# Kernel optimization log

Hardware: AMD Instinct MI355X
Metric: run time of the kernel (lower is better)

## Reference

```python
import jax, jax.numpy as jnp
import numpy as np

T, B, C, H = 2048, 2, 1024, 16
DK = C // H


def setup_inputs() -> dict:
    key = jax.random.key(0)
    ks = jax.random.split(key, 12)
    s = 1.0 / np.sqrt(C)
    return {
        "query": jax.random.normal(ks[0], (T, B, C), jnp.float32),
        "key": jax.random.normal(ks[1], (T, B, C), jnp.float32),
        "value": jax.random.normal(ks[2], (T, B, C), jnp.float32),
        "Wq": jax.random.normal(ks[3], (C, C), jnp.float32) * s,
        "bq": jnp.zeros((C,), jnp.float32),
        "Wk": jax.random.normal(ks[4], (C, C), jnp.float32) * s,
        "bk": jnp.zeros((C,), jnp.float32),
        "Wv": jax.random.normal(ks[5], (C, C), jnp.float32) * s,
        "bv": jnp.zeros((C,), jnp.float32),
        "Wo": jax.random.normal(ks[6], (C, C), jnp.float32) * s,
        "bo": jnp.zeros((C,), jnp.float32),
        "key_padding_mask": jax.random.randint(ks[7], (B, T), 0, 2).astype(jnp.bool_),
    }


def reference(query, key, value, Wq, bq, Wk, bk, Wv, bv, Wo, bo, key_padding_mask):
    # T,B,C -> B,T,C
    q_in = jnp.transpose(query, (1, 0, 2))
    k_in = jnp.transpose(key, (1, 0, 2))
    v_in = jnp.transpose(value, (1, 0, 2))
    nb = q_in.shape[0]
    # linear projections, split heads: B,T,C -> B,H,T,dk
    def proj(x, W, b):
        y = x @ W.T + b
        return jnp.transpose(y.reshape(nb, -1, H, DK), (0, 2, 1, 3))
    q = proj(q_in, Wq, bq)
    k = proj(k_in, Wk, bk)
    v = proj(v_in, Wv, bv)
    # scores: B,H,T1,T2
    scores = jnp.einsum("bhqd,bhkd->bhqk", q, k) / np.sqrt(DK).astype(np.float32)
    scores = jnp.where(key_padding_mask[:, None, None, :], -jnp.inf, scores)
    attn = jax.nn.softmax(scores, axis=-1)
    # context: B,H,T1,dk -> B,T1,C
    x = jnp.einsum("bhqk,bhkd->bhqd", attn, v)
    x = jnp.transpose(x, (0, 2, 1, 3)).reshape(nb, -1, H * DK)
    out = x @ Wo.T + bo
    # B,T,C -> T,B,C
    return jnp.transpose(out, (1, 0, 2))
```

## Files before the change

kernel.cpp:

```cpp
#include <hip/hip_runtime.h>
#include <stdint.h>

typedef __attribute__((ext_vector_type(4))) float f32x4;
typedef __attribute__((ext_vector_type(16))) float f32x16;
typedef __attribute__((ext_vector_type(8))) short bf16x8;
typedef __attribute__((ext_vector_type(2))) unsigned int u32x2;
typedef __attribute__((ext_vector_type(4))) unsigned int u32x4;
typedef unsigned short u16;
typedef unsigned int u32;

#define DEVINL __device__ __forceinline__

DEVINL u16 f2bf(float f) {
  u32 u = __builtin_bit_cast(u32, f);
  u += 0x7FFFu + ((u >> 16) & 1u);
  return (u16)(u >> 16);
}

DEVINL float exp2_hw(float x) {
  float r;
  asm("v_exp_f32 %0, %1\n\ts_nop 0" : "=v"(r) : "v"(x));
  return r;
}

DEVINL u32 cvt_pk_bf16(float lo, float hi) {
  u32 r;
  asm("v_cvt_pk_bf16_f32 %0, %1, %2" : "=v"(r) : "v"(lo), "v"(hi));
  return r;
}

DEVINL void gload16(const void* g, void* l) {
  __builtin_amdgcn_global_load_lds((const __attribute__((address_space(1))) void*)g,
                                   (__attribute__((address_space(3))) void*)l, 16, 0, 0);
}

DEVINL void wait_vm0() { asm volatile("s_waitcnt vmcnt(0)" ::: "memory"); }
DEVINL void wait_vm3() { asm volatile("s_waitcnt vmcnt(3)" ::: "memory"); }
DEVINL void wait_vm4() { asm volatile("s_waitcnt vmcnt(4)" ::: "memory"); }
DEVINL void wait_vm6() { asm volatile("s_waitcnt vmcnt(6)" ::: "memory"); }

__global__ void cvt_w_mask(const float* __restrict__ wq, const float* __restrict__ wk,
                           const float* __restrict__ wv, const float* __restrict__ wo,
                           ushort4* __restrict__ dst,
                           const u32* __restrict__ mraw, float* __restrict__ mout) {
  if (blockIdx.x == 4096) {
    __shared__ int notint, notfloat;
    int tid = threadIdx.x;
    if (tid == 0) { notint = 0; notfloat = 0; }
    __syncthreads();
    for (int i = tid; i < 1024; i += 256) {
      u32 w = mraw[i];
      if (w != 0u && w != 1u) notint = 1;
      if (w != 0u && w != 0x3f800000u) notfloat = 1;
    }
    __syncthreads();
    bool words = (!notint) || (!notfloat);
    for (int i = tid; i < 4096; i += 256) {
      u32 v = words ? mraw[i] : (u32)(((const unsigned char*)mraw)[i]);
      mout[i] = v ? -1.0e38f : -8.0f;
    }
    return;
  }
  int i = blockIdx.x * 256 + threadIdx.x;
  float4 v4;
  if (i < 262144) v4 = ((const float4*)wq)[i];
  else if (i < 524288) v4 = ((const float4*)wk)[i - 262144];
  else if (i < 786432) v4 = ((const float4*)wv)[i - 524288];
  else v4 = ((const float4*)wo)[i - 786432];
  ushort4 o;
  o.x = f2bf(v4.x); o.y = f2bf(v4.y); o.z = f2bf(v4.z); o.w = f2bf(v4.w);
  dst[i] = o;
}

DEVINL void gemm_f32a_body(const float* __restrict__ A, const u16* __restrict__ W,
                           const float* __restrict__ bias, u16* __restrict__ out_bf,
                           int tile, int mode, float scale, float* Asf, u16* Bs) {
  const int tid = threadIdx.x, lane = tid & 63;
  const int wave = tid >> 6, wm = wave & 1, wn = wave >> 1;
  const int m0 = (tile >> 3) << 7;
  const int n0 = (tile & 7) << 7;
  const int l15 = lane & 15, l4 = lane >> 4;
  const f32x4 zero = {0.f, 0.f, 0.f, 0.f};
  f32x4 acc[4][4];
#pragma unroll
  for (int i = 0; i < 4; i++)
#pragma unroll
    for (int j = 0; j < 4; j++) acc[i][j] = zero;

  auto stage = [&](int buf, int kti) {
    float* Ab = Asf + buf * 4096;
    u16* Bb = Bs + buf * 4096;
#pragma unroll
    for (int it = 0; it < 4; ++it) {
      int c = tid + (it << 8);
      int row = c >> 3, qs = (c & 7) ^ (row & 7);
      gload16(A + (size_t)(m0 + row) * 1024 + kti * 32 + qs * 4, (void*)(Ab + c * 4));
    }
#pragma unroll
    for (int it = 0; it < 2; ++it) {
      int c = tid + (it << 8);
      int row = c >> 2, qs = (c & 3) ^ ((row & 3) ^ ((row >> 2) & 3));
      gload16(W + (size_t)(n0 + row) * 1024 + kti * 32 + qs * 8, (void*)(Bb + c * 8));
    }
  };

  stage(0, 0);

  for (int kti = 0; kti < 32; ++kti) {
    if (kti < 31) stage((kti + 1) & 1, kti + 1);
    if (kti == 31) wait_vm0(); else wait_vm6();
    __builtin_amdgcn_s_barrier();
    __builtin_amdgcn_sched_barrier(0);

    const float* Ac = Asf + (kti & 1) * 4096;
    const u16* Bc = Bs + (kti & 1) * 4096;
    bf16x8 af[4], bfr[4];
#pragma unroll
    for (int i = 0; i < 4; i++) {
      int ra = (wm << 6) + (i << 4) + l15;
      int sw = ra & 7;
      float4 v0 = *(const float4*)(Ac + ra * 32 + ((((l4 << 1) | 0) ^ sw) << 2));
      float4 v1 = *(const float4*)(Ac + ra * 32 + ((((l4 << 1) | 1) ^ sw) << 2));
      u32x4 aw = {cvt_pk_bf16(v0.x, v0.y), cvt_pk_bf16(v0.z, v0.w),
                  cvt_pk_bf16(v1.x, v1.y), cvt_pk_bf16(v1.z, v1.w)};
      af[i] = __builtin_bit_cast(bf16x8, aw);
      int rb = (wn << 6) + (i << 4) + l15;
      bfr[i] = *(const bf16x8*)(Bc + rb * 32 + ((l4 * 8) ^ ((((rb & 3) ^ ((rb >> 2) & 3))) << 3)));
    }
    __builtin_amdgcn_s_setprio(1);
#pragma unroll
    for (int i = 0; i < 4; i++)
#pragma unroll
      for (int j = 0; j < 4; j++)
        acc[i][j] = __builtin_amdgcn_mfma_f32_16x16x32_bf16(af[i], bfr[j], acc[i][j], 0, 0, 0);
    __builtin_amdgcn_s_setprio(0);
    if (kti < 31) __builtin_amdgcn_s_barrier();
  }

#pragma unroll
  for (int j = 0; j < 4; j++) {
    const int col = n0 + (wn << 6) + (j << 4) + l15;
    const float bc = bias[col];
#pragma unroll
    for (int i = 0; i < 4; i++) {
#pragma unroll
      for (int r = 0; r < 4; r++) {
        const int row = m0 + (wm << 6) + (i << 4) + (l4 << 2) + r;
        float v = (acc[i][j][r] + bc) * scale;
        int t = row >> 1, b2 = row & 1, h = col >> 6, dh = col & 63;
        if (mode == 2)
          out_bf[((size_t)(b2 * 16 + h) * 64 + dh) * 2048 + t] = f2bf(v);
        else
          out_bf[((size_t)(b2 * 16 + h) * 2048 + t) * 64 + dh] = f2bf(v);
      }
    }
  }
}

__global__ __launch_bounds__(256, 3) void gemm_qkv(
    const float* __restrict__ q_in, const float* __restrict__ k_in, const float* __restrict__ v_in,
    const u16* __restrict__ wq, const u16* __restrict__ wk, const u16* __restrict__ wv,
    const float* __restrict__ bq, const float* __restrict__ bk, const float* __restrict__ bv,
    u16* __restrict__ Qh, u16* __restrict__ Kh, u16* __restrict__ Vth) {
  __shared__ __align__(16) float Asf[2 * 4096];
  __shared__ __align__(16) u16 Bs[2 * 4096];
  const float C2 = 0.18033688011112042f;
  int wg = blockIdx.x;
  int swz = (wg & 7) * 96 + (wg >> 3);
  int prob = swz >> 8, tile = swz & 255;
  if (prob == 0)      gemm_f32a_body(q_in, wq, bq, Qh,  tile, 0, C2, Asf, Bs);
  else if (prob == 1) gemm_f32a_body(k_in, wk, bk, Kh,  tile, 0, 1.0f, Asf, Bs);
  else                gemm_f32a_body(v_in, wv, bv, Vth, tile, 2, 1.0f, Asf, Bs);
}

__global__ __launch_bounds__(256, 2) void gemm_o(
    const u16* __restrict__ ctx, const u16* __restrict__ wo,
    const float* __restrict__ bo, float* __restrict__ out) {
  __shared__ __align__(16) u16 As[3 * 2048];
  __shared__ __align__(16) u16 Bs[3 * 4096];
  const int tid = threadIdx.x, lane = tid & 63;
  const int wave = tid >> 6, wm = wave & 1, wn = wave >> 1;
  const int wg = blockIdx.x;
  const int swz = (wg & 7) * 64 + (wg >> 3);
  const int m0 = (swz >> 3) << 6;
  const int n0 = (swz & 7) << 7;
  const int l15 = lane & 15, l4 = lane >> 4;
  const f32x4 zero = {0.f, 0.f, 0.f, 0.f};
  f32x4 acc[2][4];
#pragma unroll
  for (int i = 0; i < 2; i++)
#pragma unroll
    for (int j = 0; j < 4; j++) acc[i][j] = zero;

  auto stage = [&](int buf, int kti) {
    u16* Ab = As + buf * 2048;
    u16* Bb = Bs + buf * 4096;
    {
      int c = tid;
      int row = c >> 2, qs = (c & 3) ^ ((row & 3) ^ ((row >> 2) & 3));
      gload16(ctx + (size_t)(m0 + row) * 1024 + kti * 32 + qs * 8, (void*)(Ab + c * 8));
    }
#pragma unroll
    for (int it = 0; it < 2; ++it) {
      int c = tid + (it << 8);
      int row = c >> 2, qs = (c & 3) ^ ((row & 3) ^ ((row >> 2) & 3));
      gload16(wo + (size_t)(n0 + row) * 1024 + kti * 32 + qs * 8, (void*)(Bb + c * 8));
    }
  };

  stage(0, 0);
  stage(1, 1);

  for (int kti = 0; kti < 32; ++kti) {
    const int cur = kti % 3;
    if (kti == 31) wait_vm0(); else wait_vm3();
    __builtin_amdgcn_s_barrier();
    __builtin_amdgcn_sched_barrier(0);
    if (kti < 30) stage((kti + 2) % 3, kti + 2);

    const u16* Ac = As + cur * 2048;
    const u16* Bc = Bs + cur * 4096;
    bf16x8 af[2], bfr[4];
#pragma unroll
    for (int i = 0; i < 2; i++) {
      int ra = (wm << 5) + (i << 4) + l15;
      af[i] = *(const bf16x8*)(Ac + ra * 32 + ((l4 * 8) ^ ((((ra & 3) ^ ((ra >> 2) & 3))) << 3)));
    }
#pragma unroll
    for (int j = 0; j < 4; j++) {
      int rb = (wn << 6) + (j << 4) + l15;
      bfr[j] = *(const bf16x8*)(Bc + rb * 32 + ((l4 * 8) ^ ((((rb & 3) ^ ((rb >> 2) & 3))) << 3)));
    }
    __builtin_amdgcn_s_setprio(1);
#pragma unroll
    for (int i = 0; i < 2; i++)
#pragma unroll
      for (int j = 0; j < 4; j++)
        acc[i][j] = __builtin_amdgcn_mfma_f32_16x16x32_bf16(af[i], bfr[j], acc[i][j], 0, 0, 0);
    __builtin_amdgcn_s_setprio(0);
  }

#pragma unroll
  for (int j = 0; j < 4; j++) {
    const int col = n0 + (wn << 6) + (j << 4) + l15;
    const float bc = bo[col];
#pragma unroll
    for (int i = 0; i < 2; i++) {
#pragma unroll
      for (int r = 0; r < 4; r++) {
        const int row = m0 + (wm << 5) + (i << 4) + (l4 << 2) + r;
        float v = acc[i][j][r] + bc;
        int t = row & 2047, b2 = row >> 11;
        out[(size_t)(t * 2 + b2) * 1024 + col] = v;
      }
    }
  }
}

__global__ __launch_bounds__(256, 2) void attn_fwd(
    const u16* __restrict__ Qh, const u16* __restrict__ Kh, const u16* __restrict__ Vt,
    const float* __restrict__ maskf, u16* __restrict__ ctx) {
  __shared__ __align__(16) u16 Ks[3][64 * 64];
  __shared__ __align__(16) u16 Vs[3][64 * 64];
  __shared__ __align__(16) float Ml[2048];
  const int tid = threadIdx.x, lane = tid & 63, wave = tid >> 6;
  const int wg = blockIdx.x;
  const int swz = (wg & 7) * 64 + (wg >> 3);
  const int qt = swz & 15, bh = swz >> 4;
  const int bb = bh >> 4, h = bh & 15;
  const int l31 = lane & 31, hi = lane >> 5;
  const size_t kvbase = (size_t)bh * 2048 * 64;
  const int qbase = qt * 128 + wave * 32;

  gload16(maskf + bb * 2048 + tid * 4, (void*)(&Ml[tid * 4]));
  gload16(maskf + bb * 2048 + 1024 + tid * 4, (void*)(&Ml[1024 + tid * 4]));

  bf16x8 qf[4];
#pragma unroll
  for (int kc = 0; kc < 4; kc++)
    qf[kc] = *(const bf16x8*)(Qh + kvbase + (size_t)(qbase + l31) * 64 + kc * 16 + hi * 8);

  f32x16 zz;
#pragma unroll
  for (int e = 0; e < 16; e++) zz[e] = 0.f;
  f32x16 O[2];
  O[0] = zz; O[1] = zz;
  float l_ = 0.f;

  auto stage = [&](int buf, int kt) {
#pragma unroll
    for (int it = 0; it < 2; ++it) {
      int c = tid + (it << 8);
      int row = c >> 3, qs = (c & 7) ^ (row & 7);
      gload16(Kh + kvbase + (size_t)(kt * 64 + row) * 64 + qs * 8, (void*)(&Ks[buf][c * 8]));
      gload16(Vt + kvbase + (size_t)row * 2048 + kt * 64 + qs * 8, (void*)(&Vs[buf][c * 8]));
    }
  };

  stage(0, 0);
  stage(1, 1);

  for (int kt = 0; kt < 32; ++kt) {
    const int cur = kt % 3;
    if (kt == 31) wait_vm0(); else wait_vm4();
    __builtin_amdgcn_s_barrier();
    __builtin_amdgcn_sched_barrier(0);
    if (kt < 30) stage((kt + 2) % 3, kt + 2);

    f32x16 s[2];
    s[0] = zz; s[1] = zz;
    __builtin_amdgcn_s_setprio(1);
#pragma unroll
    for (int kc = 0; kc < 4; kc++) {
      const int ch = (((kc * 2 + hi) ^ (l31 & 7)) << 3);
      bf16x8 kf0 = *(const bf16x8*)(&Ks[cur][l31 * 64 + ch]);
      bf16x8 kf1 = *(const bf16x8*)(&Ks[cur][(l31 + 32) * 64 + ch]);
      s[0] = __builtin_amdgcn_mfma_f32_32x32x16_bf16(kf0, qf[kc], s[0], 0, 0, 0);
      s[1] = __builtin_amdgcn_mfma_f32_32x32x16_bf16(kf1, qf[kc], s[1], 0, 0, 0);
    }
    __builtin_amdgcn_s_setprio(0);

    float rs = 0.f;
#pragma unroll
    for (int kb = 0; kb < 2; kb++)
#pragma unroll
      for (int g = 0; g < 4; g++) {
        float4 mv = *(const float4*)(&Ml[kt * 64 + kb * 32 + g * 8 + hi * 4]);
        float p0 = exp2_hw(s[kb][4 * g + 0] + mv.x);
        float p1 = exp2_hw(s[kb][4 * g + 1] + mv.y);
        float p2 = exp2_hw(s[kb][4 * g + 2] + mv.z);
        float p3 = exp2_hw(s[kb][4 * g + 3] + mv.w);
        s[kb][4 * g + 0] = p0; s[kb][4 * g + 1] = p1;
        s[kb][4 * g + 2] = p2; s[kb][4 * g + 3] = p3;
        rs += (p0 + p1) + (p2 + p3);
      }
    rs += __shfl_xor(rs, 32);
    l_ += rs;

    u32 pw[2][8];
#pragma unroll
    for (int kb = 0; kb < 2; kb++)
#pragma unroll
      for (int g = 0; g < 4; g++) {
        pw[kb][2 * g]     = cvt_pk_bf16(s[kb][4 * g + 0], s[kb][4 * g + 1]);
        pw[kb][2 * g + 1] = cvt_pk_bf16(s[kb][4 * g + 2], s[kb][4 * g + 3]);
      }

    __builtin_amdgcn_s_setprio(1);
#pragma unroll
    for (int kc = 0; kc < 4; kc++) {
      const int kb = kc >> 1, m = kc & 1;
      auto r0 = __builtin_amdgcn_permlane32_swap(pw[kb][4 * m + 0], pw[kb][4 * m + 2], false, false);
      auto r1 = __builtin_amdgcn_permlane32_swap(pw[kb][4 * m + 1], pw[kb][4 * m + 3], false, false);
      u32x4 fw = {r0[0], r1[0], r0[1], r1[1]};
      bf16x8 pf = __builtin_bit_cast(bf16x8, fw);
      const int ch = (((kc * 2 + hi) ^ (l31 & 7)) << 3);
      bf16x8 vf0 = *(const bf16x8*)(&Vs[cur][l31 * 64 + ch]);
      bf16x8 vf1 = *(const bf16x8*)(&Vs[cur][(l31 + 32) * 64 + ch]);
      O[0] = __builtin_amdgcn_mfma_f32_32x32x16_bf16(vf0, pf, O[0], 0, 0, 0);
      O[1] = __builtin_amdgcn_mfma_f32_32x32x16_bf16(vf1, pf, O[1], 0, 0, 0);
    }
    __builtin_amdgcn_s_setprio(0);
  }

  float inv = (l_ > 0.f) ? 1.0f / l_ : 0.f;
  const int q = qbase + l31;
  u16* cb = ctx + ((size_t)bb * 2048 + q) * 1024 + h * 64;
#pragma unroll
  for (int nd = 0; nd < 2; nd++)
#pragma unroll
    for (int g = 0; g < 4; g++) {
      u32x2 w;
      w[0] = cvt_pk_bf16(O[nd][4 * g + 0] * inv, O[nd][4 * g + 1] * inv);
      w[1] = cvt_pk_bf16(O[nd][4 * g + 2] * inv, O[nd][4 * g + 3] * inv);
      *(u32x2*)(cb + nd * 32 + g * 8 + hi * 4) = w;
    }
}

extern "C" void kernel_launch(void* const* d_in, const int* in_sizes, int n_in,
                              void* d_out, int out_size, void* d_ws, size_t ws_size,
                              hipStream_t stream) {
  const float* q_in = (const float*)d_in[0];
  const float* k_in = (const float*)d_in[1];
  const float* v_in = (const float*)d_in[2];
  const float* Wq = (const float*)d_in[3];
  const float* bq = (const float*)d_in[4];
  const float* Wk = (const float*)d_in[5];
  const float* bk = (const float*)d_in[6];
  const float* Wv = (const float*)d_in[7];
  const float* bv = (const float*)d_in[8];
  const float* Wo = (const float*)d_in[9];
  const float* bo = (const float*)d_in[10];
  const void* mask = d_in[11];

  const size_t SZ_X = (size_t)4194304 * 2;
  const size_t SZ_W = (size_t)1048576 * 2;
  uint8_t* ws = (uint8_t*)d_ws;
  float* mf = (float*)ws;
  size_t off = 32768;
  u16* wqb = (u16*)(ws + off); off += SZ_W;
  u16* wkb = (u16*)(ws + off); off += SZ_W;
  u16* wvb = (u16*)(ws + off); off += SZ_W;
  u16* wob = (u16*)(ws + off); off += SZ_W;
  u16* Qh  = (u16*)(ws + off); off += SZ_X;
  u16* Kh  = (u16*)(ws + off); off += SZ_X;
  u16* Vth = (u16*)(ws + off); off += SZ_X;
  u16* ctx = (u16*)(ws + off); off += SZ_X;
  if (ws_size < off) return;

  cvt_w_mask<<<4097, 256, 0, stream>>>(Wq, Wk, Wv, Wo, (ushort4*)wqb, (const u32*)mask, mf);

  gemm_qkv<<<768, 256, 0, stream>>>(q_in, k_in, v_in, wqb, wkb, wvb, bq, bk, bv, Qh, Kh, Vth);

  attn_fwd<<<512, 256, 0, stream>>>(Qh, Kh, Vth, mf, ctx);

  gemm_o<<<512, 256, 0, stream>>>(ctx, wob, bo, (float*)d_out);
}
```

Measured before the change: 128.3 us.

## Convert QKV GEMM A tiles to bf16 in registers before LDS, triple-buffered

The fused QKV projection GEMM now loads the fp32 activation tile into registers rather than copying it straight into LDS. It converts it to bf16 once and writes the packed result into swizzled LDS, using a three-stage buffer for both operands. Before, every wave read fp32 from LDS and repeated the conversion, which doubled LDS read traffic for A. The cost is more register pressure and a register-staged pipeline with manual waitcnt handling; one `wait_vm8` is written without a call and does nothing.

```diff
diff --git a/kernel.cpp b/kernel.cpp
--- a/kernel.cpp
+++ b/kernel.cpp
@@ -35,9 +35,12 @@
 }
 
 DEVINL void wait_vm0() { asm volatile("s_waitcnt vmcnt(0)" ::: "memory"); }
+DEVINL void wait_vm2() { asm volatile("s_waitcnt vmcnt(2)" ::: "memory"); }
 DEVINL void wait_vm3() { asm volatile("s_waitcnt vmcnt(3)" ::: "memory"); }
 DEVINL void wait_vm4() { asm volatile("s_waitcnt vmcnt(4)" ::: "memory"); }
-DEVINL void wait_vm6() { asm volatile("s_waitcnt vmcnt(6)" ::: "memory"); }
+DEVINL void wait_vm8() { asm volatile("s_waitcnt vmcnt(8)" ::: "memory"); }
+DEVINL void wait_lgkm0() { asm volatile("s_waitcnt lgkmcnt(0)" ::: "memory"); }
+#define SBAR0 __builtin_amdgcn_sched_barrier(0)
 
 __global__ void cvt_w_mask(const float* __restrict__ wq, const float* __restrict__ wk,
                            const float* __restrict__ wv, const float* __restrict__ wo,
@@ -74,7 +77,7 @@
 
 DEVINL void gemm_f32a_body(const float* __restrict__ A, const u16* __restrict__ W,
                            const float* __restrict__ bias, u16* __restrict__ out_bf,
-                           int tile, int mode, float scale, float* Asf, u16* Bs) {
+                           int tile, int mode, float scale, u16* As, u16* Bs) {
   const int tid = threadIdx.x, lane = tid & 63;
   const int wave = tid >> 6, wm = wave & 1, wn = wave >> 1;
   const int m0 = (tile >> 3) << 7;
@@ -87,15 +90,18 @@
 #pragma unroll
     for (int j = 0; j < 4; j++) acc[i][j] = zero;
 
-  auto stage = [&](int buf, int kti) {
-    float* Ab = Asf + buf * 4096;
+  const int arow = tid >> 1, ahalf = tid & 1;
+  const float* Abase = A + (size_t)(m0 + arow) * 1024 + ahalf * 16;
+  const int asw = (arow & 3) ^ ((arow >> 2) & 3);
+
+  auto issueA = [&](float4 (&rld)[4], int kti) {
+#pragma unroll
+    for (int i = 0; i < 4; i++)
+      rld[i] = *(const float4*)(Abase + kti * 32 + 4 * i);
+    SBAR0;
+  };
+  auto issueB = [&](int buf, int kti) {
     u16* Bb = Bs + buf * 4096;
-#pragma unroll
-    for (int it = 0; it < 4; ++it) {
-      int c = tid + (it << 8);
-      int row = c >> 3, qs = (c & 7) ^ (row & 7);
-      gload16(A + (size_t)(m0 + row) * 1024 + kti * 32 + qs * 4, (void*)(Ab + c * 4));
-    }
 #pragma unroll
     for (int it = 0; it < 2; ++it) {
       int c = tid + (it << 8);
@@ -103,28 +109,27 @@
       gload16(W + (size_t)(n0 + row) * 1024 + kti * 32 + qs * 8, (void*)(Bb + c * 8));
     }
   };
-
-  stage(0, 0);
-
-  for (int kti = 0; kti < 32; ++kti) {
-    if (kti < 31) stage((kti + 1) & 1, kti + 1);
-    if (kti == 31) wait_vm0(); else wait_vm6();
-    __builtin_amdgcn_s_barrier();
-    __builtin_amdgcn_sched_barrier(0);
-
-    const float* Ac = Asf + (kti & 1) * 4096;
-    const u16* Bc = Bs + (kti & 1) * 4096;
+  auto cvtwrite = [&](float4 (&rcv)[4], int buf) {
+    u16* Ab = As + buf * 4096;
+#pragma unroll
+    for (int j = 0; j < 2; j++) {
+      u32x4 w = {cvt_pk_bf16(rcv[2 * j].x, rcv[2 * j].y),
+                 cvt_pk_bf16(rcv[2 * j].z, rcv[2 * j].w),
+                 cvt_pk_bf16(rcv[2 * j + 1].x, rcv[2 * j + 1].y),
+                 cvt_pk_bf16(rcv[2 * j + 1].z, rcv[2 * j + 1].w)};
+      int chunk = ahalf * 2 + j;
+      *(u32x4*)(Ab + arow * 32 + ((chunk ^ asw) << 3)) = w;
+    }
+  };
+  auto compute = [&](int cur) {
+    const u16* Ac = As + cur * 4096;
+    const u16* Bc = Bs + cur * 4096;
     bf16x8 af[4], bfr[4];
 #pragma unroll
     for (int i = 0; i < 4; i++) {
       int ra = (wm << 6) + (i << 4) + l15;
-      int sw = ra & 7;
-      float4 v0 = *(const float4*)(Ac + ra * 32 + ((((l4 << 1) | 0) ^ sw) << 2));
-      float4 v1 = *(const float4*)(Ac + ra * 32 + ((((l4 << 1) | 1) ^ sw) << 2));
-      u32x4 aw = {cvt_pk_bf16(v0.x, v0.y), cvt_pk_bf16(v0.z, v0.w),
-                  cvt_pk_bf16(v1.x, v1.y), cvt_pk_bf16(v1.z, v1.w)};
-      af[i] = __builtin_bit_cast(bf16x8, aw);
       int rb = (wn << 6) + (i << 4) + l15;
+      af[i]  = *(const bf16x8*)(Ac + ra * 32 + ((l4 * 8) ^ ((((ra & 3) ^ ((ra >> 2) & 3))) << 3)));
       bfr[i] = *(const bf16x8*)(Bc + rb * 32 + ((l4 * 8) ^ ((((rb & 3) ^ ((rb >> 2) & 3))) << 3)));
     }
     __builtin_amdgcn_s_setprio(1);
@@ -134,7 +139,28 @@
       for (int j = 0; j < 4; j++)
         acc[i][j] = __builtin_amdgcn_mfma_f32_16x16x32_bf16(af[i], bfr[j], acc[i][j], 0, 0, 0);
     __builtin_amdgcn_s_setprio(0);
-    if (kti < 31) __builtin_amdgcn_s_barrier();
+  };
+
+  float4 regs0[4], regs1[4];
+  issueA(regs0, 0); issueB(0, 0);
+  issueA(regs1, 1); issueB(1, 1);
+  wait_vm8; SBAR0;
+  cvtwrite(regs0, 0);
+
+  auto iter = [&](int kti, float4 (&rcv)[4], float4 (&rld)[4]) {
+    if (kti == 31) wait_vm0(); else wait_vm2();
+    SBAR0;
+    if (kti < 31) cvtwrite(rcv, (kti + 1) % 3);
+    wait_lgkm0();
+    SBAR0;
+    __builtin_amdgcn_s_barrier();
+    if (kti < 30) { issueA(rld, kti + 2); issueB((kti + 2) % 3, kti + 2); }
+    compute(kti % 3);
+  };
+
+  for (int kp = 0; kp < 16; ++kp) {
+    iter(2 * kp, regs1, regs0);
+    iter(2 * kp + 1, regs0, regs1);
   }
 
 #pragma unroll
@@ -162,15 +188,15 @@
     const u16* __restrict__ wq, const u16* __restrict__ wk, const u16* __restrict__ wv,
     const float* __restrict__ bq, const float* __restrict__ bk, const float* __restrict__ bv,
     u16* __restrict__ Qh, u16* __restrict__ Kh, u16* __restrict__ Vth) {
-  __shared__ __align__(16) float Asf[2 * 4096];
-  __shared__ __align__(16) u16 Bs[2 * 4096];
+  __shared__ __align__(16) u16 As[3 * 4096];
+  __shared__ __align__(16) u16 Bs[3 * 4096];
   const float C2 = 0.18033688011112042f;
   int wg = blockIdx.x;
   int swz = (wg & 7) * 96 + (wg >> 3);
   int prob = swz >> 8, tile = swz & 255;
-  if (prob == 0)      gemm_f32a_body(q_in, wq, bq, Qh,  tile, 0, C2, Asf, Bs);
-  else if (prob == 1) gemm_f32a_body(k_in, wk, bk, Kh,  tile, 0, 1.0f, Asf, Bs);
-  else                gemm_f32a_body(v_in, wv, bv, Vth, tile, 2, 1.0f, Asf, Bs);
+  if (prob == 0)      gemm_f32a_body(q_in, wq, bq, Qh,  tile, 0, C2, As, Bs);
+  else if (prob == 1) gemm_f32a_body(k_in, wk, bk, Kh,  tile, 0, 1.0f, As, Bs);
+  else                gemm_f32a_body(v_in, wv, bv, Vth, tile, 2, 1.0f, As, Bs);
 }
 
 __global__ __launch_bounds__(256, 2) void gemm_o(
@@ -215,7 +241,7 @@
     const int cur = kti % 3;
     if (kti == 31) wait_vm0(); else wait_vm3();
     __builtin_amdgcn_s_barrier();
-    __builtin_amdgcn_sched_barrier(0);
+    SBAR0;
     if (kti < 30) stage((kti + 2) % 3, kti + 2);
 
     const u16* Ac = As + cur * 2048;
@@ -304,7 +330,7 @@
     const int cur = kt % 3;
     if (kt == 31) wait_vm0(); else wait_vm4();
     __builtin_amdgcn_s_barrier();
-    __builtin_amdgcn_sched_barrier(0);
+    SBAR0;
     if (kt < 30) stage((kt + 2) % 3, kt + 2);
 
     f32x16 s[2];
```

Result: slower. 135.0 us (+5.2%).

## Pre-convert QKV activations to bf16 and triple-buffer the QKV GEMM

Applied to the files above, without the earlier changes.

The conversion kernel now also casts the query, key and value activations to bf16 in workspace, alongside the weights. The QKV GEMM then loads bf16 A tiles directly instead of fp32 tiles that were converted in registers. This halves the A-tile LDS footprint, which allows a three-stage pipeline with one barrier per iteration instead of double buffering with two. The cost is an extra pass that reads 48MB of fp32 and writes 24MB of bf16 before the GEMM, trading in-GEMM conversion and load traffic for a separate memory-bound kernel.

```diff
diff --git a/kernel.cpp b/kernel.cpp
--- a/kernel.cpp
+++ b/kernel.cpp
@@ -37,13 +37,14 @@
 DEVINL void wait_vm0() { asm volatile("s_waitcnt vmcnt(0)" ::: "memory"); }
 DEVINL void wait_vm3() { asm volatile("s_waitcnt vmcnt(3)" ::: "memory"); }
 DEVINL void wait_vm4() { asm volatile("s_waitcnt vmcnt(4)" ::: "memory"); }
-DEVINL void wait_vm6() { asm volatile("s_waitcnt vmcnt(6)" ::: "memory"); }
-
-__global__ void cvt_w_mask(const float* __restrict__ wq, const float* __restrict__ wk,
-                           const float* __restrict__ wv, const float* __restrict__ wo,
-                           ushort4* __restrict__ dst,
-                           const u32* __restrict__ mraw, float* __restrict__ mout) {
-  if (blockIdx.x == 4096) {
+#define SBAR0 __builtin_amdgcn_sched_barrier(0)
+
+__global__ void cvt_all(const float* __restrict__ q, const float* __restrict__ k,
+                        const float* __restrict__ v, const float* __restrict__ wq,
+                        const float* __restrict__ wk, const float* __restrict__ wv,
+                        const float* __restrict__ wo, ushort4* __restrict__ dst,
+                        const u32* __restrict__ mraw, float* __restrict__ mout) {
+  if (blockIdx.x == 16384) {
     __shared__ int notint, notfloat;
     int tid = threadIdx.x;
     if (tid == 0) { notint = 0; notfloat = 0; }
@@ -56,30 +57,37 @@
     __syncthreads();
     bool words = (!notint) || (!notfloat);
     for (int i = tid; i < 4096; i += 256) {
-      u32 v = words ? mraw[i] : (u32)(((const unsigned char*)mraw)[i]);
-      mout[i] = v ? -1.0e38f : -8.0f;
+      u32 vv = words ? mraw[i] : (u32)(((const unsigned char*)mraw)[i]);
+      mout[i] = vv ? -1.0e38f : -8.0f;
     }
     return;
   }
   int i = blockIdx.x * 256 + threadIdx.x;
   float4 v4;
-  if (i < 262144) v4 = ((const float4*)wq)[i];
-  else if (i < 524288) v4 = ((const float4*)wk)[i - 262144];
-  else if (i < 786432) v4 = ((const float4*)wv)[i - 524288];
-  else v4 = ((const float4*)wo)[i - 786432];
+  if (i < 1048576) v4 = ((const float4*)q)[i];
+  else if (i < 2097152) v4 = ((const float4*)k)[i - 1048576];
+  else if (i < 3145728) v4 = ((const float4*)v)[i - 2097152];
+  else {
+    int j = i - 3145728;
+    if (j < 262144) v4 = ((const float4*)wq)[j];
+    else if (j < 524288) v4 = ((const float4*)wk)[j - 262144];
+    else if (j < 786432) v4 = ((const float4*)wv)[j - 524288];
+    else v4 = ((const float4*)wo)[j - 786432];
+  }
   ushort4 o;
   o.x = f2bf(v4.x); o.y = f2bf(v4.y); o.z = f2bf(v4.z); o.w = f2bf(v4.w);
   dst[i] = o;
 }
 
-DEVINL void gemm_f32a_body(const float* __restrict__ A, const u16* __restrict__ W,
-                           const float* __restrict__ bias, u16* __restrict__ out_bf,
-                           int tile, int mode, float scale, float* Asf, u16* Bs) {
+DEVINL void gemm_body(const u16* __restrict__ A, const u16* __restrict__ W,
+                      const float* __restrict__ bias, u16* __restrict__ out_bf,
+                      int tile, int mode, float scale, u16* As, u16* Bs) {
   const int tid = threadIdx.x, lane = tid & 63;
   const int wave = tid >> 6, wm = wave & 1, wn = wave >> 1;
   const int m0 = (tile >> 3) << 7;
   const int n0 = (tile & 7) << 7;
   const int l15 = lane & 15, l4 = lane >> 4;
+  const int K = 1024;
   const f32x4 zero = {0.f, 0.f, 0.f, 0.f};
   f32x4 acc[4][4];
 #pragma unroll
@@ -88,43 +96,35 @@
     for (int j = 0; j < 4; j++) acc[i][j] = zero;
 
   auto stage = [&](int buf, int kti) {
-    float* Ab = Asf + buf * 4096;
+    u16* Ab = As + buf * 4096;
     u16* Bb = Bs + buf * 4096;
-#pragma unroll
-    for (int it = 0; it < 4; ++it) {
-      int c = tid + (it << 8);
-      int row = c >> 3, qs = (c & 7) ^ (row & 7);
-      gload16(A + (size_t)(m0 + row) * 1024 + kti * 32 + qs * 4, (void*)(Ab + c * 4));
-    }
 #pragma unroll
     for (int it = 0; it < 2; ++it) {
       int c = tid + (it << 8);
       int row = c >> 2, qs = (c & 3) ^ ((row & 3) ^ ((row >> 2) & 3));
-      gload16(W + (size_t)(n0 + row) * 1024 + kti * 32 + qs * 8, (void*)(Bb + c * 8));
+      gload16(A + (size_t)(m0 + row) * K + kti * 32 + qs * 8, (void*)(Ab + c * 8));
+      gload16(W + (size_t)(n0 + row) * K + kti * 32 + qs * 8, (void*)(Bb + c * 8));
     }
   };
 
   stage(0, 0);
+  stage(1, 1);
 
   for (int kti = 0; kti < 32; ++kti) {
-    if (kti < 31) stage((kti + 1) & 1, kti + 1);
-    if (kti == 31) wait_vm0(); else wait_vm6();
+    const int cur = kti % 3;
+    if (kti == 31) wait_vm0(); else wait_vm4();
     __builtin_amdgcn_s_barrier();
-    __builtin_amdgcn_sched_barrier(0);
-
-    const float* Ac = Asf + (kti & 1) * 4096;
-    const u16* Bc = Bs + (kti & 1) * 4096;
+    SBAR0;
+    if (kti < 30) stage((kti + 2) % 3, kti + 2);
+
+    const u16* Ac = As + cur * 4096;
+    const u16* Bc = Bs + cur * 4096;
     bf16x8 af[4], bfr[4];
 #pragma unroll
     for (int i = 0; i < 4; i++) {
       int ra = (wm << 6) + (i << 4) + l15;
-      int sw = ra & 7;
-      float4 v0 = *(const float4*)(Ac + ra * 32 + ((((l4 << 1) | 0) ^ sw) << 2));
-      float4 v1 = *(const float4*)(Ac + ra * 32 + ((((l4 << 1) | 1) ^ sw) << 2));
-      u32x4 aw = {cvt_pk_bf16(v0.x, v0.y), cvt_pk_bf16(v0.z, v0.w),
-                  cvt_pk_bf16(v1.x, v1.y), cvt_pk_bf16(v1.z, v1.w)};
-      af[i] = __builtin_bit_cast(bf16x8, aw);
       int rb = (wn << 6) + (i << 4) + l15;
+      af[i]  = *(const bf16x8*)(Ac + ra * 32 + ((l4 * 8) ^ ((((ra & 3) ^ ((ra >> 2) & 3))) << 3)));
       bfr[i] = *(const bf16x8*)(Bc + rb * 32 + ((l4 * 8) ^ ((((rb & 3) ^ ((rb >> 2) & 3))) << 3)));
     }
     __builtin_amdgcn_s_setprio(1);
@@ -134,7 +134,6 @@
       for (int j = 0; j < 4; j++)
         acc[i][j] = __builtin_amdgcn_mfma_f32_16x16x32_bf16(af[i], bfr[j], acc[i][j], 0, 0, 0);
     __builtin_amdgcn_s_setprio(0);
-    if (kti < 31) __builtin_amdgcn_s_barrier();
   }
 
 #pragma unroll
@@ -158,19 +157,19 @@
 }
 
 __global__ __launch_bounds__(256, 3) void gemm_qkv(
-    const float* __restrict__ q_in, const float* __restrict__ k_in, const float* __restrict__ v_in,
+    const u16* __restrict__ qbf, const u16* __restrict__ kbf, const u16* __restrict__ vbf,
     const u16* __restrict__ wq, const u16* __restrict__ wk, const u16* __restrict__ wv,
     const float* __restrict__ bq, const float* __restrict__ bk, const float* __restrict__ bv,
     u16* __restrict__ Qh, u16* __restrict__ Kh, u16* __restrict__ Vth) {
-  __shared__ __align__(16) float Asf[2 * 4096];
-  __shared__ __align__(16) u16 Bs[2 * 4096];
+  __shared__ __align__(16) u16 As[3 * 4096];
+  __shared__ __align__(16) u16 Bs[3 * 4096];
   const float C2 = 0.18033688011112042f;
   int wg = blockIdx.x;
   int swz = (wg & 7) * 96 + (wg >> 3);
   int prob = swz >> 8, tile = swz & 255;
-  if (prob == 0)      gemm_f32a_body(q_in, wq, bq, Qh,  tile, 0, C2, Asf, Bs);
-  else if (prob == 1) gemm_f32a_body(k_in, wk, bk, Kh,  tile, 0, 1.0f, Asf, Bs);
-  else                gemm_f32a_body(v_in, wv, bv, Vth, tile, 2, 1.0f, Asf, Bs);
+  if (prob == 0)      gemm_body(qbf, wq, bq, Qh,  tile, 0, C2, As, Bs);
+  else if (prob == 1) gemm_body(kbf, wk, bk, Kh,  tile, 0, 1.0f, As, Bs);
+  else                gemm_body(vbf, wv, bv, Vth, tile, 2, 1.0f, As, Bs);
 }
 
 __global__ __launch_bounds__(256, 2) void gemm_o(
@@ -215,7 +214,7 @@
     const int cur = kti % 3;
     if (kti == 31) wait_vm0(); else wait_vm3();
     __builtin_amdgcn_s_barrier();
-    __builtin_amdgcn_sched_barrier(0);
+    SBAR0;
     if (kti < 30) stage((kti + 2) % 3, kti + 2);
 
     const u16* Ac = As + cur * 2048;
@@ -304,7 +303,7 @@
     const int cur = kt % 3;
     if (kt == 31) wait_vm0(); else wait_vm4();
     __builtin_amdgcn_s_barrier();
-    __builtin_amdgcn_sched_barrier(0);
+    SBAR0;
     if (kt < 30) stage((kt + 2) % 3, kt + 2);
 
     f32x16 s[2];
@@ -398,6 +397,9 @@
   uint8_t* ws = (uint8_t*)d_ws;
   float* mf = (float*)ws;
   size_t off = 32768;
+  u16* qbf = (u16*)(ws + off); off += SZ_X;
+  u16* kbf = (u16*)(ws + off); off += SZ_X;
+  u16* vbf = (u16*)(ws + off); off += SZ_X;
   u16* wqb = (u16*)(ws + off); off += SZ_W;
   u16* wkb = (u16*)(ws + off); off += SZ_W;
   u16* wvb = (u16*)(ws + off); off += SZ_W;
@@ -408,9 +410,10 @@
   u16* ctx = (u16*)(ws + off); off += SZ_X;
   if (ws_size < off) return;
 
-  cvt_w_mask<<<4097, 256, 0, stream>>>(Wq, Wk, Wv, Wo, (ushort4*)wqb, (const u32*)mask, mf);
-
-  gemm_qkv<<<768, 256, 0, stream>>>(q_in, k_in, v_in, wqb, wkb, wvb, bq, bk, bv, Qh, Kh, Vth);
+  cvt_all<<<16385, 256, 0, stream>>>(q_in, k_in, v_in, Wq, Wk, Wv, Wo,
+                                     (ushort4*)qbf, (const u32*)mask, mf);
+
+  gemm_qkv<<<768, 256, 0, stream>>>(qbf, kbf, vbf, wqb, wkb, wvb, bq, bk, bv, Qh, Kh, Vth);
 
   attn_fwd<<<512, 256, 0, stream>>>(Qh, Kh, Vth, mf, ctx);
 
```

Result: slower. 134.8 us (+5.0%).
